# Optimization experiments

Measured on AMD Instinct MI355X. Metric: run time of the kernel, lower is better.

Reference implementation:

```python
import jax, jax.numpy as jnp
import numpy as np

B, N, C = 8, 4096, 256
HEADS, SR = 8, 4
LN_EPS = 1e-5

def setup_inputs() -> dict:
    key = jax.random.key(0)
    ks = jax.random.split(key, 8)
    std = 0.02
    x = jax.random.normal(ks[0], (B, N, C), dtype=jnp.float32)
    q_w = jax.random.normal(ks[1], (C, C), dtype=jnp.float32) * std          # [in,out]
    kv_w = jax.random.normal(ks[2], (C, 2 * C), dtype=jnp.float32) * std     # [in,2*out]
    fan_out = SR * SR * C
    sr_w = jax.random.normal(ks[3], (C, C, SR, SR), dtype=jnp.float32) * np.sqrt(2.0 / fan_out)  # OIHW
    sr_b = jnp.zeros((C,), dtype=jnp.float32)
    ln_w = jnp.ones((C,), dtype=jnp.float32)
    ln_b = jnp.zeros((C,), dtype=jnp.float32)
    proj_w = jax.random.normal(ks[4], (C, C), dtype=jnp.float32) * std
    proj_b = jnp.zeros((C,), dtype=jnp.float32)
    return {"x": x, "H": 64, "W": 64, "q_w": q_w, "kv_w": kv_w, "sr_w": sr_w,
            "sr_b": sr_b, "ln_w": ln_w, "ln_b": ln_b, "proj_w": proj_w, "proj_b": proj_b}


def reference(x, H, W, q_w, kv_w, sr_w, sr_b, ln_w, ln_b, proj_w, proj_b):
    Bb, Nn, Cc = x.shape
    hd = Cc // HEADS
    scale = hd ** -0.5
    # q: [B, heads, N, hd]
    q = (x @ q_w).reshape(Bb, Nn, HEADS, hd).transpose(0, 2, 1, 3)
    # spatial reduction: conv(stride=sr) + LayerNorm
    x_ = x.transpose(0, 2, 1).reshape(Bb, Cc, H, W)
    x_ = jax.lax.conv_general_dilated(
        x_, sr_w, window_strides=(SR, SR), padding="VALID",
        dimension_numbers=("NCHW", "OIHW", "NCHW")) + sr_b[None, :, None, None]
    x_ = x_.reshape(Bb, Cc, -1).transpose(0, 2, 1)  # [B, Nk, C]
    mu = x_.mean(-1, keepdims=True)
    var = x_.var(-1, keepdims=True)
    x_ = (x_ - mu) * jax.lax.rsqrt(var + LN_EPS) * ln_w + ln_b
    # kv: [B, Nk, 2, heads, hd]
    Nk = x_.shape[1]
    kv = (x_ @ kv_w).reshape(Bb, Nk, 2, HEADS, hd)
    k = kv[:, :, 0].transpose(0, 2, 1, 3)  # [B, heads, Nk, hd]
    v = kv[:, :, 1].transpose(0, 2, 1, 3)  # [B, heads, Nk, hd]
    attn = jnp.einsum("bhnd,bhmd->bhnm", q, k) * scale
    attn = jax.nn.softmax(attn, axis=-1)
    out = jnp.einsum("bhnm,bhmd->bhnd", attn, v)  # [B, heads, N, hd]
    out = out.transpose(0, 2, 1, 3).reshape(Bb, Nn, Cc)
    return out @ proj_w + proj_b
```

## Files before the change

kernel.cpp:

```cpp
#include <hip/hip_runtime.h>
#include <hip/hip_bf16.h>
#include <math.h>

#define DI __device__ __forceinline__

static constexpr float SCALE = 0.17677669529663687f;

typedef short bf16x8 __attribute__((ext_vector_type(8)));
typedef float f32x4 __attribute__((ext_vector_type(4)));

__device__ unsigned short g_qw2[(size_t)256 * 8 * 64];
__device__ unsigned short g_kvw2[(size_t)512 * 8 * 64];
__device__ unsigned short g_pw2[(size_t)256 * 8 * 64];
__device__ unsigned short g_wt2[(size_t)256 * 128 * 64];
__device__ unsigned short g_x2[(size_t)32768 * 8 * 64];
__device__ unsigned short g_ln2[(size_t)2048 * 8 * 64];
__device__ unsigned short g_q[(size_t)64 * 4096 * 32];
__device__ unsigned short g_k[(size_t)64 * 256 * 32];
__device__ unsigned short g_vt[(size_t)64 * 32 * 256];
__device__ unsigned short g_convp[(size_t)16 * 2048 * 256];
__device__ unsigned short g_attnb[(size_t)32768 * 256];

DI float bfbits2f(unsigned short b) { return __uint_as_float(((unsigned)b) << 16); }

DI unsigned short f2bf(float f) {
  unsigned u = __float_as_uint(f);
  unsigned r = (u + 0x7fffu + ((u >> 16) & 1u)) >> 16;
  return (unsigned short)r;
}

DI float4 ld_bf4(const unsigned short* p) {
  ushort4 u = *(const ushort4*)p;
  return make_float4(bfbits2f(u.x), bfbits2f(u.y), bfbits2f(u.z), bfbits2f(u.w));
}

DI float ld1(const void* p, size_t i, int f32) {
  return f32 ? ((const float*)p)[i] : bfbits2f(((const unsigned short*)p)[i]);
}

DI float4 ld4(const void* p, size_t i, int f32) {
  if (f32) return *(const float4*)((const float*)p + i);
  return ld_bf4((const unsigned short*)p + i);
}

typedef const __attribute__((address_space(1))) void* gas_p;
typedef __attribute__((address_space(3))) void* las_p;
DI void gload16(const unsigned short* g, short* l) {
  __builtin_amdgcn_global_load_lds((gas_p)g, (las_p)l, 16, 0, 0);
}

template <int N> DI void wait_vmcnt() {
  if constexpr (N == 6) asm volatile("s_waitcnt vmcnt(6)" ::: "memory");
  else if constexpr (N == 5) asm volatile("s_waitcnt vmcnt(5)" ::: "memory");
  else if constexpr (N == 4) asm volatile("s_waitcnt vmcnt(4)" ::: "memory");
  else asm volatile("s_waitcnt vmcnt(0)" ::: "memory");
}

DI int detect_f32(const void* xp) {
  const unsigned* p = (const unsigned*)xp;
  unsigned m0 = 0, m1 = 0;
#pragma unroll
  for (int i = 0; i < 32; ++i) {
    unsigned w = p[i];
    unsigned lo = w & 0x7fffu, hi = (w >> 16) & 0x7fffu;
    m0 = lo > m0 ? lo : m0;
    m1 = hi > m1 ? hi : m1;
  }
  unsigned mm = m0 > m1 ? m0 : m1;
  return mm >= 0x4680u ? 1 : 0;
}

__global__ void k_prep(const void* __restrict__ qw, const void* __restrict__ kvw,
                       const void* __restrict__ pwp, const void* __restrict__ srw,
                       const void* __restrict__ xp) {
  const int f32 = detect_f32(xp);
  int tidg = blockIdx.x * 256 + threadIdx.x;
  float v[8];
  unsigned short* dst;
  if (tidg < 8192) {
    int o = tidg >> 5, w = tidg & 31, k = w * 8;
#pragma unroll
    for (int j = 0; j < 8; ++j) v[j] = ld1(qw, (size_t)(k + j) * 256 + o, f32) * SCALE;
    dst = g_qw2 + ((size_t)o * 8 + (w >> 2)) * 64 + (w & 3) * 8;
  } else if (tidg < 24576) {
    int t = tidg - 8192;
    int o = t >> 5, w = t & 31, k = w * 8;
#pragma unroll
    for (int j = 0; j < 8; ++j) v[j] = ld1(kvw, (size_t)(k + j) * 512 + o, f32);
    dst = g_kvw2 + ((size_t)o * 8 + (w >> 2)) * 64 + (w & 3) * 8;
  } else if (tidg < 32768) {
    int t = tidg - 24576;
    int o = t >> 5, w = t & 31, k = w * 8;
#pragma unroll
    for (int j = 0; j < 8; ++j) v[j] = ld1(pwp, (size_t)(k + j) * 256 + o, f32);
    dst = g_pw2 + ((size_t)o * 8 + (w >> 2)) * 64 + (w & 3) * 8;
  } else if (tidg < 163840) {
    int t = tidg - 32768;
    int o = t >> 9, w = t & 511, k = w * 8;
#pragma unroll
    for (int j = 0; j < 8; ++j) {
      int kk = k + j, tap = kk >> 8, ci = kk & 255;
      v[j] = ld1(srw, (size_t)o * 4096 + (size_t)ci * 16 + tap, f32);
    }
    dst = g_wt2 + ((size_t)o * 128 + (w >> 2)) * 64 + (w & 3) * 8;
  } else {
    int t = tidg - 163840;
    int m = t >> 5, w = t & 31, k = w * 8;
    size_t base = (size_t)m * 256 + k;
    float4 a = ld4(xp, base, f32);
    float4 b = ld4(xp, base + 4, f32);
    v[0] = a.x; v[1] = a.y; v[2] = a.z; v[3] = a.w;
    v[4] = b.x; v[5] = b.y; v[6] = b.z; v[7] = b.w;
    dst = g_x2 + ((size_t)m * 8 + (w >> 2)) * 64 + (w & 3) * 8;
  }
  ushort4 h0, h1, l0, l1;
  h0.x = f2bf(v[0]); l0.x = f2bf(v[0] - bfbits2f(h0.x));
  h0.y = f2bf(v[1]); l0.y = f2bf(v[1] - bfbits2f(h0.y));
  h0.z = f2bf(v[2]); l0.z = f2bf(v[2] - bfbits2f(h0.z));
  h0.w = f2bf(v[3]); l0.w = f2bf(v[3] - bfbits2f(h0.w));
  h1.x = f2bf(v[4]); l1.x = f2bf(v[4] - bfbits2f(h1.x));
  h1.y = f2bf(v[5]); l1.y = f2bf(v[5] - bfbits2f(h1.y));
  h1.z = f2bf(v[6]); l1.z = f2bf(v[6] - bfbits2f(h1.z));
  h1.w = f2bf(v[7]); l1.w = f2bf(v[7] - bfbits2f(h1.w));
  *(ushort4*)dst        = h0;
  *(ushort4*)(dst + 4)  = h1;
  *(ushort4*)(dst + 32) = l0;
  *(ushort4*)(dst + 36) = l1;
}

template <int MODE>
DI void mgemm_body(short* smem, int bx, int nblk, int z,
                   const void* __restrict__ biasp, void* __restrict__ outp, int f32) {
  constexpr bool AH = (MODE != 3);
  constexpr int BN  = (MODE == 2) ? 64 : 128;
  constexpr int NJ  = BN / 64;
  constexpr int NBR = BN / 32;
  constexpr int ASZ = AH ? 4096 : 2048;
  constexpr int BSZ = NBR * 2048;
  constexpr int BUF = ASZ + BSZ;
  constexpr int NLD = (AH ? 2 : 1) + NBR;
  constexpr int NIT = (MODE == 1) ? 32 : 8;
  constexpr int NKT = (MODE == 1) ? 128 : 8;

  const int tid = threadIdx.x;
  const int m0 = bx * 64;
  const int wave = tid >> 6, lane = tid & 63;
  const int quad = lane >> 4, l15 = lane & 15;

  const int srow = tid >> 3;
  const int slot = (tid & 7) ^ (srow & 7);

  size_t arow0 = 0, arow1 = 0, abase3 = 0;
  if constexpr (MODE == 0 || MODE == 2) {
    arow0 = m0 + srow;
    arow1 = m0 + 32 + srow;
  } else if constexpr (MODE == 1) {
#pragma unroll
    for (int r = 0; r < 2; ++r) {
      int m = m0 + r * 32 + srow;
      int bb = m >> 8, sp = m & 255;
      int oh = sp >> 4, ow = sp & 15;
      size_t rb = (size_t)bb * 4096 + (4 * oh + z) * 64 + 4 * ow;
      if (r == 0) arow0 = rb; else arow1 = rb;
    }
  } else {
    int ar = tid >> 2;
    int s3 = (tid & 3) ^ (ar & 3);
    abase3 = (size_t)(m0 + ar) * 256 + s3 * 8;
  }

  const unsigned short* Asrc =
      (MODE == 0 || MODE == 1) ? g_x2 : (MODE == 2) ? g_ln2 : g_attnb;
  const unsigned short* Bsrc = (MODE == 0) ? g_qw2 : (MODE == 1) ? g_wt2
                             : (MODE == 2) ? g_kvw2 : g_pw2;
  const int brow0 = nblk * BN + srow;

  int aoff[4], boff[NJ];
#pragma unroll
  for (int mt = 0; mt < 4; ++mt) {
    int ar = mt * 16 + l15;
    if constexpr (AH) aoff[mt] = ar * 64 + ((quad ^ (ar & 7)) << 3);
    else              aoff[mt] = ar * 32 + ((quad ^ (ar & 3)) << 3);
  }
#pragma unroll
  for (int j = 0; j < NJ; ++j) {
    int br = wave * (16 * NJ) + j * 16 + l15;
    boff[j] = br * 64 + ((quad ^ (br & 7)) << 3);
  }

  auto STAGE = [&](int it, int b) {
    short* sa = smem + b * BUF;
    short* sb = sa + ASZ;
    if constexpr (MODE == 0 || MODE == 2) {
      gload16(Asrc + (arow0 * 8 + it) * 64 + slot * 8, sa + tid * 8);
      gload16(Asrc + (arow1 * 8 + it) * 64 + slot * 8, sa + 2048 + tid * 8);
    } else if constexpr (MODE == 1) {
      const int kw = it >> 3, ktA = it & 7;
      gload16(Asrc + ((arow0 + kw) * 8 + ktA) * 64 + slot * 8, sa + tid * 8);
      gload16(Asrc + ((arow1 + kw) * 8 + ktA) * 64 + slot * 8, sa + 2048 + tid * 8);
    } else {
      gload16(Asrc + abase3 + (size_t)it * 32, sa + tid * 8);
    }
    const int ktB = (MODE == 1) ? (z * 32 + it) : it;
#pragma unroll
    for (int r = 0; r < NBR; ++r)
      gload16(Bsrc + ((size_t)(brow0 + r * 32) * NKT + ktB) * 64 + slot * 8,
              sb + tid * 8 + r * 2048);
  };

  f32x4 acc[4][NJ] = {};

  auto COMPUTE = [&](int cur) {
    const short* sa = smem + cur * BUF;
    const short* sb = sa + ASZ;
#pragma unroll
    for (int mt = 0; mt < 4; ++mt) {
      bf16x8 a_h = *(const bf16x8*)&sa[aoff[mt]];
      bf16x8 a_l;
      if constexpr (AH) a_l = *(const bf16x8*)&sa[aoff[mt] ^ 32];
#pragma unroll
      for (int j = 0; j < NJ; ++j) {
        bf16x8 b_h = *(const bf16x8*)&sb[boff[j]];
        bf16x8 b_l = *(const bf16x8*)&sb[boff[j] ^ 32];
        f32x4 c = acc[mt][j];
        c = __builtin_amdgcn_mfma_f32_16x16x32_bf16(a_h, b_h, c, 0, 0, 0);
        if constexpr (AH)
          c = __builtin_amdgcn_mfma_f32_16x16x32_bf16(a_l, b_h, c, 0, 0, 0);
        c = __builtin_amdgcn_mfma_f32_16x16x32_bf16(a_h, b_l, c, 0, 0, 0);
        acc[mt][j] = c;
      }
    }
  };

  STAGE(0, 0);
  STAGE(1, 1);
#pragma unroll 1
  for (int it = 0; it < NIT - 1; ++it) {
    const int cur = it & 1;
    wait_vmcnt<NLD>();
    __builtin_amdgcn_s_barrier();
    __builtin_amdgcn_sched_barrier(0);
    COMPUTE(cur);
    asm volatile("" ::: "memory");
    __builtin_amdgcn_s_barrier();
    __builtin_amdgcn_sched_barrier(0);
    if (it < NIT - 2) STAGE(it + 2, cur);
  }
  wait_vmcnt<0>();
  __builtin_amdgcn_s_barrier();
  __builtin_amdgcn_sched_barrier(0);
  COMPUTE((NIT - 1) & 1);

  const int f32o = f32;
#pragma unroll
  for (int mt = 0; mt < 4; ++mt) {
#pragma unroll
    for (int j = 0; j < NJ; ++j) {
#pragma unroll
      for (int r = 0; r < 4; ++r) {
        int m = m0 + mt * 16 + quad * 4 + r;
        int c = nblk * BN + wave * (16 * NJ) + j * 16 + l15;
        float v = acc[mt][j][r];
        if constexpr (MODE == 0) {
          int b = m >> 12, n = m & 4095;
          int h = c >> 5, d = c & 31;
          g_q[(((size_t)(b * 8 + h) * 4096 + n) << 5) + d] = f2bf(v);
        } else if constexpr (MODE == 1) {
          g_convp[((size_t)z * 2048 + m) * 256 + c] = f2bf(v);
        } else if constexpr (MODE == 2) {
          int s = c >> 8, h = (c >> 5) & 7, d = c & 31;
          int bb = m >> 8, nk = m & 255;
          if (s == 0) {
            g_k[(((size_t)(bb * 8 + h) * 256 + nk) << 5) + d] = f2bf(v);
          } else {
            int w = nk & 31, cb = nk & ~31;
            int ww = w & 15;
            int vslot = cb + ((ww >> 2) << 3) + ((w >> 4) << 2) + (ww & 3);
            g_vt[(((size_t)(bb * 8 + h) * 32 + d) << 8) + vslot] = f2bf(v);
          }
        } else {
          float rr = v + ld1(biasp, c, f32o);
          if (f32o) ((float*)outp)[(size_t)m * 256 + c] = rr;
          else      ((unsigned short*)outp)[(size_t)m * 256 + c] = f2bf(rr);
        }
      }
    }
  }
}

__launch_bounds__(256, 3)
__global__ void k_mgemm01() {
  __shared__ __align__(16) short smem[2 * 12288];
  int bid = blockIdx.x;
  if (bid < 256) {
    int m = bid & 31, nb = (bid >> 5) & 1, z = bid >> 6;
    mgemm_body<1>(smem, m, nb, z, nullptr, nullptr, 0);
  } else {
    int bq = bid - 256;
    int lq = (bq & 7) * 128 + (bq >> 3);
    mgemm_body<0>(smem, lq >> 1, lq & 1, 0, nullptr, nullptr, 0);
  }
}

__launch_bounds__(256, 3)
__global__ void k_mgemm2() {
  __shared__ __align__(16) short smem[2 * 8192];
  int b = blockIdx.x;
  int lq = (b & 7) * 32 + (b >> 3);
  mgemm_body<2>(smem, lq >> 3, lq & 7, 0, nullptr, nullptr, 0);
}

__global__ void k_redln(const void* __restrict__ xp, const void* __restrict__ srb,
                        const void* __restrict__ lw, const void* __restrict__ lb) {
  const int f32 = detect_f32(xp);
  const int t = threadIdx.x;
  const int row = blockIdx.x * 8 + (t >> 5);
  const int l32 = t & 31;
  const int ch0 = l32 * 8;
  const size_t idx = (size_t)row * 256 + ch0;

  float c[8] = {};
#pragma unroll
  for (int zz = 0; zz < 4; ++zz) {
    uint4 u = *(const uint4*)&g_convp[(size_t)zz * (2048 * 256) + idx];
    c[0] += __uint_as_float(u.x << 16); c[1] += __uint_as_float(u.x & 0xffff0000u);
    c[2] += __uint_as_float(u.y << 16); c[3] += __uint_as_float(u.y & 0xffff0000u);
    c[4] += __uint_as_float(u.z << 16); c[5] += __uint_as_float(u.z & 0xffff0000u);
    c[6] += __uint_as_float(u.w << 16); c[7] += __uint_as_float(u.w & 0xffff0000u);
  }
  float4 b0 = ld4(srb, ch0, f32), b1 = ld4(srb, ch0 + 4, f32);
  c[0] += b0.x; c[1] += b0.y; c[2] += b0.z; c[3] += b0.w;
  c[4] += b1.x; c[5] += b1.y; c[6] += b1.z; c[7] += b1.w;

  float s = 0.f, sq = 0.f;
#pragma unroll
  for (int j = 0; j < 8; ++j) { s += c[j]; sq += c[j] * c[j]; }
#pragma unroll
  for (int off = 16; off >= 1; off >>= 1) {
    s += __shfl_xor(s, off, 32);
    sq += __shfl_xor(sq, off, 32);
  }
  float mu = s * (1.0f / 256.0f);
  float var = sq * (1.0f / 256.0f) - mu * mu;
  float rr = rsqrtf(var + 1e-5f);

  float4 w0 = ld4(lw, ch0, f32), w1 = ld4(lw, ch0 + 4, f32);
  float4 e0 = ld4(lb, ch0, f32), e1 = ld4(lb, ch0 + 4, f32);
  float wv[8] = {w0.x, w0.y, w0.z, w0.w, w1.x, w1.y, w1.z, w1.w};
  float ev[8] = {e0.x, e0.y, e0.z, e0.w, e1.x, e1.y, e1.z, e1.w};

  float o[8];
#pragma unroll
  for (int j = 0; j < 8; ++j) o[j] = (c[j] - mu) * rr * wv[j] + ev[j];

  ushort4 h0, h1, l0, l1;
  h0.x = f2bf(o[0]); l0.x = f2bf(o[0] - bfbits2f(h0.x));
  h0.y = f2bf(o[1]); l0.y = f2bf(o[1] - bfbits2f(h0.y));
  h0.z = f2bf(o[2]); l0.z = f2bf(o[2] - bfbits2f(h0.z));
  h0.w = f2bf(o[3]); l0.w = f2bf(o[3] - bfbits2f(h0.w));
  h1.x = f2bf(o[4]); l1.x = f2bf(o[4] - bfbits2f(h1.x));
  h1.y = f2bf(o[5]); l1.y = f2bf(o[5] - bfbits2f(h1.y));
  h1.z = f2bf(o[6]); l1.z = f2bf(o[6] - bfbits2f(h1.z));
  h1.w = f2bf(o[7]); l1.w = f2bf(o[7] - bfbits2f(h1.w));

  const size_t dbase = ((size_t)row * 8 + (l32 >> 2)) * 64 + (l32 & 3) * 8;
  *(ushort4*)&g_ln2[dbase]          = h0;
  *(ushort4*)&g_ln2[dbase + 4]      = h1;
  *(ushort4*)&g_ln2[dbase + 32]     = l0;
  *(ushort4*)&g_ln2[dbase + 36]     = l1;
}

__launch_bounds__(256, 2)
__global__ void k_attnproj(const void* __restrict__ xp, const void* __restrict__ pb,
                           void* __restrict__ outp) {
  __shared__ __align__(16) short smem[16384 + 18688];
  short* att = smem;
  short* skv = smem + 16384;

  const int f32o = detect_f32(xp);
  const int tid = threadIdx.x;
  int lq = ((int)blockIdx.x & 7) * 64 + ((int)blockIdx.x >> 3);
  const int b = lq >> 6, ntile = lq & 63;

  const int wave = tid >> 6, lane = tid & 63;
  const int quad = lane >> 4, l15 = lane & 15;
  const int rw = wave * 16 + l15;
  const int n0g = ntile * 64 + wave * 16;

  short* sk  = skv;
  short* svt = skv + 10240;

#pragma unroll 1
  for (int h = 0; h < 8; ++h) {
    const int bh = b * 8 + h;
    {
      const uint4* gk = (const uint4*)(g_k + (size_t)bh * 8192);
      const uint4* gv = (const uint4*)(g_vt + (size_t)bh * 8192);
      for (int i = tid; i < 1024; i += 256) {
        int key = i >> 2, part = i & 3;
        *(uint4*)&sk[key * 40 + part * 8] = gk[i];
        int d = i >> 5, off = (i & 31) * 8;
        *(uint4*)&svt[d * 264 + off] = gv[i];
      }
    }
    __syncthreads();

    bf16x8 qv = *(const bf16x8*)(g_q + ((size_t)bh * 4096 + n0g + l15) * 32 + quad * 8);

    f32x4 sacc[16];
    __builtin_amdgcn_s_setprio(1);
#pragma unroll
    for (int t = 0; t < 16; ++t) {
      bf16x8 kf = *(const bf16x8*)&sk[(t * 16 + l15) * 40 + quad * 8];
      f32x4 c = {0.f, 0.f, 0.f, 0.f};
      sacc[t] = __builtin_amdgcn_mfma_f32_16x16x32_bf16(kf, qv, c, 0, 0, 0);
    }
    __builtin_amdgcn_s_setprio(0);

    float m = sacc[0][0];
#pragma unroll
    for (int t = 0; t < 16; ++t) {
#pragma unroll
      for (int r = 0; r < 4; ++r) m = fmaxf(m, sacc[t][r]);
    }
    m = fmaxf(m, __shfl_xor(m, 16, 64));
    m = fmaxf(m, __shfl_xor(m, 32, 64));

    unsigned plo[16], phi[16];
    float ls = 0.f;
#pragma unroll
    for (int t = 0; t < 16; ++t) {
      unsigned short p0 = f2bf(__expf(sacc[t][0] - m));
      unsigned short p1 = f2bf(__expf(sacc[t][1] - m));
      unsigned short p2 = f2bf(__expf(sacc[t][2] - m));
      unsigned short p3 = f2bf(__expf(sacc[t][3] - m));
      ls += bfbits2f(p0) + bfbits2f(p1) + bfbits2f(p2) + bfbits2f(p3);
      plo[t] = (unsigned)p0 | ((unsigned)p1 << 16);
      phi[t] = (unsigned)p2 | ((unsigned)p3 << 16);
    }
    ls += __shfl_xor(ls, 16, 64);
    ls += __shfl_xor(ls, 32, 64);
    float inv = 1.0f / ls;

    f32x4 o0 = {0.f, 0.f, 0.f, 0.f}, o1 = {0.f, 0.f, 0.f, 0.f};
    __builtin_amdgcn_s_setprio(1);
#pragma unroll
    for (int c = 0; c < 8; ++c) {
      uint4 pk = make_uint4(plo[2 * c], phi[2 * c], plo[2 * c + 1], phi[2 * c + 1]);
      bf16x8 pf = *(bf16x8*)&pk;
      bf16x8 v0 = *(const bf16x8*)&svt[l15 * 264 + c * 32 + quad * 8];
      bf16x8 v1 = *(const bf16x8*)&svt[(16 + l15) * 264 + c * 32 + quad * 8];
      o0 = __builtin_amdgcn_mfma_f32_16x16x32_bf16(v0, pf, o0, 0, 0, 0);
      o1 = __builtin_amdgcn_mfma_f32_16x16x32_bf16(v1, pf, o1, 0, 0, 0);
    }
    __builtin_amdgcn_s_setprio(0);

    ushort4 u0, u1;
    u0.x = f2bf(o0[0] * inv); u0.y = f2bf(o0[1] * inv);
    u0.z = f2bf(o0[2] * inv); u0.w = f2bf(o0[3] * inv);
    u1.x = f2bf(o1[0] * inv); u1.y = f2bf(o1[1] * inv);
    u1.z = f2bf(o1[2] * inv); u1.w = f2bf(o1[3] * inv);
    int s0 = h * 4 + (quad >> 1);
    int woff = (quad & 1) * 4;
    *(ushort4*)&att[rw * 256 + (((s0    ) ^ (rw & 7)) << 3) + woff] = u0;
    *(ushort4*)&att[rw * 256 + (((s0 + 2) ^ (rw & 7)) << 3) + woff] = u1;
    __syncthreads();
  }

  const int srow = tid >> 3;
  const int slot = (tid & 7) ^ (srow & 7);

  auto STAGE_B = [&](int s) {
    short* sb = skv + (s & 1) * 8192;
    int nb = s >> 3, it = s & 7;
    int brow0 = nb * 128 + srow;
#pragma unroll
    for (int r = 0; r < 4; ++r)
      gload16(g_pw2 + ((size_t)(brow0 + r * 32) * 8 + it) * 64 + slot * 8,
              sb + tid * 8 + r * 2048);
  };

  int boff[2];
#pragma unroll
  for (int j = 0; j < 2; ++j) {
    int br = wave * 32 + j * 16 + l15;
    boff[j] = br * 64 + ((quad ^ (br & 7)) << 3);
  }

  f32x4 acc[4][2] = {};

  auto PCOMP = [&](int s) {
    const short* sb = skv + (s & 1) * 8192;
    int it = s & 7;
#pragma unroll
    for (int mt = 0; mt < 4; ++mt) {
      int ar = mt * 16 + l15;
      bf16x8 a_h = *(const bf16x8*)&att[ar * 256 + (((it * 4 + quad) ^ (ar & 7)) << 3)];
#pragma unroll
      for (int j = 0; j < 2; ++j) {
        bf16x8 b_h = *(const bf16x8*)&sb[boff[j]];
        bf16x8 b_l = *(const bf16x8*)&sb[boff[j] ^ 32];
        f32x4 c = acc[mt][j];
        c = __builtin_amdgcn_mfma_f32_16x16x32_bf16(a_h, b_h, c, 0, 0, 0);
        c = __builtin_amdgcn_mfma_f32_16x16x32_bf16(a_h, b_l, c, 0, 0, 0);
        acc[mt][j] = c;
      }
    }
  };

  auto EPI = [&](int nb) {
#pragma unroll
    for (int mt = 0; mt < 4; ++mt) {
#pragma unroll
      for (int j = 0; j < 2; ++j) {
#pragma unroll
        for (int r = 0; r < 4; ++r) {
          int m = ntile * 64 + mt * 16 + quad * 4 + r;
          int c = nb * 128 + wave * 32 + j * 16 + l15;
          float v = acc[mt][j][r] + ld1(pb, c, f32o);
          if (f32o) ((float*)outp)[((size_t)b * 4096 + m) * 256 + c] = v;
          else ((unsigned short*)outp)[((size_t)b * 4096 + m) * 256 + c] = f2bf(v);
          acc[mt][j][r] = 0.f;
        }
      }
    }
  };

  STAGE_B(0);
  STAGE_B(1);
#pragma unroll 1
  for (int s = 0; s < 15; ++s) {
    wait_vmcnt<4>();
    __builtin_amdgcn_s_barrier();
    __builtin_amdgcn_sched_barrier(0);
    PCOMP(s);
    asm volatile("" ::: "memory");
    __builtin_amdgcn_s_barrier();
    __builtin_amdgcn_sched_barrier(0);
    if (s < 14) STAGE_B(s + 2);
    if (s == 7) EPI(0);
  }
  wait_vmcnt<0>();
  __builtin_amdgcn_s_barrier();
  __builtin_amdgcn_sched_barrier(0);
  PCOMP(15);
  EPI(1);
}

extern "C" void kernel_launch(void* const* d_in, const int* in_sizes, int n_in,
                              void* d_out, int out_size, void* d_ws, size_t ws_size,
                              hipStream_t stream) {
  const void* x   = d_in[0];
  const void* qw  = d_in[3];
  const void* kvw = d_in[4];
  const void* srw = d_in[5];
  const void* srb = d_in[6];
  const void* lnw = d_in[7];
  const void* lnb = d_in[8];
  const void* pw  = d_in[9];
  const void* pb  = d_in[10];

  k_prep<<<4736, 256, 0, stream>>>(qw, kvw, pw, srw, x);
  k_mgemm01<<<1280, 256, 0, stream>>>();
  k_redln<<<256, 256, 0, stream>>>(x, srb, lnw, lnb);
  k_mgemm2<<<256, 256, 0, stream>>>();
  k_attnproj<<<512, 256, 0, stream>>>(x, pb, d_out);
}
```

Baseline: 202.1 us.

## Prefetch next head's K/V/Q into registers and split projection accumulators

In the fused attention+projection kernel, the next head's K, V^T and Q fragments are loaded from global memory into registers while the current head's softmax and PV run. They are written to LDS after a barrier, so load latency overlaps with compute instead of stalling at the top of each head iteration. The projection phase also keeps two accumulator sets (one per 128-column half), which moves the first-half epilogue stores out of the middle of the pipelined loop to the end. This raises register pressure (eight uint4 prefetch registers plus a second accumulator array), which could reduce occupancy or cause spills.

```diff
diff --git a/kernel.cpp b/kernel.cpp
--- a/kernel.cpp
+++ b/kernel.cpp
@@ -390,22 +390,23 @@
   short* sk  = skv;
   short* svt = skv + 10240;
 
+  {
+    const uint4* gk = (const uint4*)(g_k + (size_t)(b * 8) * 8192);
+    const uint4* gv = (const uint4*)(g_vt + (size_t)(b * 8) * 8192);
+    for (int i = tid; i < 1024; i += 256) {
+      int key = i >> 2, part = i & 3;
+      *(uint4*)&sk[key * 40 + part * 8] = gk[i];
+      int d = i >> 5, off = (i & 31) * 8;
+      *(uint4*)&svt[d * 264 + off] = gv[i];
+    }
+  }
+  __syncthreads();
+
+  bf16x8 qv = *(const bf16x8*)(g_q + ((size_t)(b * 8) * 4096 + n0g + l15) * 32 + quad * 8);
+
 #pragma unroll 1
   for (int h = 0; h < 8; ++h) {
     const int bh = b * 8 + h;
-    {
-      const uint4* gk = (const uint4*)(g_k + (size_t)bh * 8192);
-      const uint4* gv = (const uint4*)(g_vt + (size_t)bh * 8192);
-      for (int i = tid; i < 1024; i += 256) {
-        int key = i >> 2, part = i & 3;
-        *(uint4*)&sk[key * 40 + part * 8] = gk[i];
-        int d = i >> 5, off = (i & 31) * 8;
-        *(uint4*)&svt[d * 264 + off] = gv[i];
-      }
-    }
-    __syncthreads();
-
-    bf16x8 qv = *(const bf16x8*)(g_q + ((size_t)bh * 4096 + n0g + l15) * 32 + quad * 8);
 
     f32x4 sacc[16];
     __builtin_amdgcn_s_setprio(1);
@@ -416,6 +417,18 @@
       sacc[t] = __builtin_amdgcn_mfma_f32_16x16x32_bf16(kf, qv, c, 0, 0, 0);
     }
     __builtin_amdgcn_s_setprio(0);
+
+    uint4 kreg0, kreg1, kreg2, kreg3, vreg0, vreg1, vreg2, vreg3;
+    bf16x8 qvn;
+    if (h < 7) {
+      const uint4* gk = (const uint4*)(g_k + (size_t)(bh + 1) * 8192);
+      const uint4* gv = (const uint4*)(g_vt + (size_t)(bh + 1) * 8192);
+      kreg0 = gk[tid];       vreg0 = gv[tid];
+      kreg1 = gk[tid + 256]; vreg1 = gv[tid + 256];
+      kreg2 = gk[tid + 512]; vreg2 = gv[tid + 512];
+      kreg3 = gk[tid + 768]; vreg3 = gv[tid + 768];
+      qvn = *(const bf16x8*)(g_q + ((size_t)(bh + 1) * 4096 + n0g + l15) * 32 + quad * 8);
+    }
 
     float m = sacc[0][0];
 #pragma unroll
@@ -464,7 +477,29 @@
     int woff = (quad & 1) * 4;
     *(ushort4*)&att[rw * 256 + (((s0    ) ^ (rw & 7)) << 3) + woff] = u0;
     *(ushort4*)&att[rw * 256 + (((s0 + 2) ^ (rw & 7)) << 3) + woff] = u1;
-    __syncthreads();
+
+    if (h < 7) {
+      __syncthreads();
+      {
+        int key = tid >> 2, part = tid & 3;
+        *(uint4*)&sk[key * 40 + part * 8] = kreg0;
+        int key1 = (tid + 256) >> 2;
+        *(uint4*)&sk[key1 * 40 + part * 8] = kreg1;
+        int key2 = (tid + 512) >> 2;
+        *(uint4*)&sk[key2 * 40 + part * 8] = kreg2;
+        int key3 = (tid + 768) >> 2;
+        *(uint4*)&sk[key3 * 40 + part * 8] = kreg3;
+        int d0 = tid >> 5, off = (tid & 31) * 8;
+        *(uint4*)&svt[d0 * 264 + off] = vreg0;
+        *(uint4*)&svt[(d0 + 8) * 264 + off] = vreg1;
+        *(uint4*)&svt[(d0 + 16) * 264 + off] = vreg2;
+        *(uint4*)&svt[(d0 + 24) * 264 + off] = vreg3;
+      }
+      qv = qvn;
+      __syncthreads();
+    } else {
+      __syncthreads();
+    }
   }
 
   const int srow = tid >> 3;
@@ -487,9 +522,10 @@
     boff[j] = br * 64 + ((quad ^ (br & 7)) << 3);
   }
 
-  f32x4 acc[4][2] = {};
-
-  auto PCOMP = [&](int s) {
+  f32x4 accA[4][2] = {};
+  f32x4 accB[4][2] = {};
+
+  auto PCOMP = [&](f32x4 (&acc)[4][2], int s) {
     const short* sb = skv + (s & 1) * 8192;
     int it = s & 7;
 #pragma unroll
@@ -508,43 +544,52 @@
     }
   };
 
-  auto EPI = [&](int nb) {
-#pragma unroll
-    for (int mt = 0; mt < 4; ++mt) {
-#pragma unroll
-      for (int j = 0; j < 2; ++j) {
-#pragma unroll
-        for (int r = 0; r < 4; ++r) {
-          int m = ntile * 64 + mt * 16 + quad * 4 + r;
-          int c = nb * 128 + wave * 32 + j * 16 + l15;
-          float v = acc[mt][j][r] + ld1(pb, c, f32o);
-          if (f32o) ((float*)outp)[((size_t)b * 4096 + m) * 256 + c] = v;
-          else ((unsigned short*)outp)[((size_t)b * 4096 + m) * 256 + c] = f2bf(v);
-          acc[mt][j][r] = 0.f;
-        }
-      }
-    }
-  };
-
   STAGE_B(0);
   STAGE_B(1);
 #pragma unroll 1
-  for (int s = 0; s < 15; ++s) {
+  for (int s = 0; s < 8; ++s) {
     wait_vmcnt<4>();
     __builtin_amdgcn_s_barrier();
     __builtin_amdgcn_sched_barrier(0);
-    PCOMP(s);
+    PCOMP(accA, s);
+    asm volatile("" ::: "memory");
+    __builtin_amdgcn_s_barrier();
+    __builtin_amdgcn_sched_barrier(0);
+    STAGE_B(s + 2);
+  }
+#pragma unroll 1
+  for (int s = 8; s < 15; ++s) {
+    wait_vmcnt<4>();
+    __builtin_amdgcn_s_barrier();
+    __builtin_amdgcn_sched_barrier(0);
+    PCOMP(accB, s);
     asm volatile("" ::: "memory");
     __builtin_amdgcn_s_barrier();
     __builtin_amdgcn_sched_barrier(0);
     if (s < 14) STAGE_B(s + 2);
-    if (s == 7) EPI(0);
   }
   wait_vmcnt<0>();
   __builtin_amdgcn_s_barrier();
   __builtin_amdgcn_sched_barrier(0);
-  PCOMP(15);
-  EPI(1);
+  PCOMP(accB, 15);
+
+#pragma unroll
+  for (int nb = 0; nb < 2; ++nb) {
+#pragma unroll
+    for (int mt = 0; mt < 4; ++mt) {
+#pragma unroll
+      for (int j = 0; j < 2; ++j) {
+#pragma unroll
+        for (int r = 0; r < 4; ++r) {
+          int m = ntile * 64 + mt * 16 + quad * 4 + r;
+          int c = nb * 128 + wave * 32 + j * 16 + l15;
+          float v = (nb == 0 ? accA[mt][j][r] : accB[mt][j][r]) + ld1(pb, c, f32o);
+          if (f32o) ((float*)outp)[((size_t)b * 4096 + m) * 256 + c] = v;
+          else ((unsigned short*)outp)[((size_t)b * 4096 + m) * 256 + c] = f2bf(v);
+        }
+      }
+    }
+  }
 }
 
 extern "C" void kernel_launch(void* const* d_in, const int* in_sizes, int n_in,
```

Result: no change. 199.3 us, median of 4 (-1.4%).
